# Performance work log

Measured on AMD Instinct MI355X. Metric: run time of the kernel, lower is better.

## Reference

```python
import jax, jax.numpy as jnp
import numpy as np

N_NODES = 100000


def gcn_conv(x, W, b, edge_index, n_nodes):
    # PyG GCNConv (default args): add self-loops, symmetric normalization,
    # linear transform first, then normalized scatter-add aggregation, then bias.
    h = x @ W  # [N, out]
    loop = jnp.arange(n_nodes, dtype=edge_index.dtype)
    row = jnp.concatenate([edge_index[0], loop])  # sources
    col = jnp.concatenate([edge_index[1], loop])  # targets
    deg = jax.ops.segment_sum(jnp.ones_like(col, dtype=h.dtype), col, num_segments=n_nodes)
    dinv = jnp.where(deg > 0, jax.lax.rsqrt(deg), 0.0)
    norm = dinv[row] * dinv[col]  # [E']
    msg = h[row] * norm[:, None]  # gather + scale
    out = jax.ops.segment_sum(msg, col, num_segments=n_nodes)  # scatter-add
    return out + b


def setup_inputs() -> dict:
    key = jax.random.key(0)
    k1, k2, k3, k4 = jax.random.split(key, 4)
    N, E, F, H, C = N_NODES, 3200000, 128, 16, 8
    x = jax.random.normal(k1, (N, F), dtype=jnp.float32)
    edge_index = jax.random.randint(k2, (2, E), 0, N, dtype=jnp.int64)
    W1 = jax.random.normal(k3, (F, H), dtype=jnp.float32) / np.sqrt(F)
    b1 = jnp.zeros((H,), dtype=jnp.float32)
    W2 = jax.random.normal(k4, (H, C), dtype=jnp.float32) / np.sqrt(H)
    b2 = jnp.zeros((C,), dtype=jnp.float32)
    return {"x": x, "edge_index": edge_index, "W1": W1, "b1": b1, "W2": W2, "b2": b2}


def reference(x, edge_index, W1, b1, W2, b2):
    n = x.shape[0]
    h = jax.nn.relu(gcn_conv(x, W1, b1, edge_index, n))
    # F.dropout(training=self.training) is identity in eval mode
    out = gcn_conv(h, W2, b2, edge_index, n)
    return jax.nn.log_softmax(out, axis=1)
```

## Files before the change

kernel.cpp:

```cpp
#include <hip/hip_runtime.h>
#include <hip/hip_fp16.h>

#define F_IN 128
#define H1   16
#define C2   8
#define BSHIFT 7
#define BNODES 128
#define MAXBUCK 1024
#define NBLK 256
#define CAP  6144
#define CHUNK_CAP 12800

__global__ __launch_bounds__(512) void binScatter2_kernel(
        const int* __restrict__ ei, int E, int chunk, int nbuck,
        int* __restrict__ bbcScan, int* __restrict__ stage) {
    __shared__ int h[MAXBUCK];
    __shared__ int sc[512];
    __shared__ unsigned short rnk[CHUNK_CAP];
    int t = threadIdx.x;
    int blk = blockIdx.x;
    int base = blk * chunk;
    int csize = max(0, min(chunk, E - base));
    int blkBase = base;

    for (int i = t; i < MAXBUCK; i += 512) h[i] = 0;
    __syncthreads();

    const int* colp = ei + E + base;
    const int* rowp = ei + base;
    bool al4 = ((E & 3) == 0) && ((base & 3) == 0) && ((csize & 3) == 0);
    bool fit = (csize <= CHUNK_CAP);

    if (al4) {
        const int4* cv = reinterpret_cast<const int4*>(colp);
        int nv = csize >> 2;
        if (fit) {
            for (int i = t; i < nv; i += 512) {
                int4 c4 = cv[i];
                rnk[4 * i + 0] = (unsigned short)atomicAdd(&h[c4.x >> BSHIFT], 1);
                rnk[4 * i + 1] = (unsigned short)atomicAdd(&h[c4.y >> BSHIFT], 1);
                rnk[4 * i + 2] = (unsigned short)atomicAdd(&h[c4.z >> BSHIFT], 1);
                rnk[4 * i + 3] = (unsigned short)atomicAdd(&h[c4.w >> BSHIFT], 1);
            }
        } else {
            for (int i = t; i < nv; i += 512) {
                int4 c4 = cv[i];
                atomicAdd(&h[c4.x >> BSHIFT], 1);
                atomicAdd(&h[c4.y >> BSHIFT], 1);
                atomicAdd(&h[c4.z >> BSHIFT], 1);
                atomicAdd(&h[c4.w >> BSHIFT], 1);
            }
        }
    } else {
        if (fit) {
            for (int i = t; i < csize; i += 512)
                rnk[i] = (unsigned short)atomicAdd(&h[colp[i] >> BSHIFT], 1);
        } else {
            for (int i = t; i < csize; i += 512) atomicAdd(&h[colp[i] >> BSHIFT], 1);
        }
    }
    __syncthreads();

    int e0 = h[2 * t], e1 = h[2 * t + 1];
    int psum = e0 + e1;
    sc[t] = psum;
    __syncthreads();
    for (int off = 1; off < 512; off <<= 1) {
        int tmp = (t >= off) ? sc[t - off] : 0;
        __syncthreads();
        sc[t] += tmp;
        __syncthreads();
    }
    int excl = sc[t] - psum;
    h[2 * t] = blkBase + excl;
    h[2 * t + 1] = blkBase + excl + e0;
    __syncthreads();

    for (int b = t; b < nbuck; b += 512)
        bbcScan[blk * nbuck + b] = h[b];
    __syncthreads();

    if (al4) {
        const int4* cv = reinterpret_cast<const int4*>(colp);
        const int4* rv = reinterpret_cast<const int4*>(rowp);
        int nv = csize >> 2;
        if (fit) {
            for (int i = t; i < nv; i += 512) {
                int4 c4 = cv[i];
                int4 r4 = rv[i];
                stage[h[c4.x >> BSHIFT] + (int)rnk[4 * i + 0]] = (r4.x << BSHIFT) | (c4.x & (BNODES - 1));
                stage[h[c4.y >> BSHIFT] + (int)rnk[4 * i + 1]] = (r4.y << BSHIFT) | (c4.y & (BNODES - 1));
                stage[h[c4.z >> BSHIFT] + (int)rnk[4 * i + 2]] = (r4.z << BSHIFT) | (c4.z & (BNODES - 1));
                stage[h[c4.w >> BSHIFT] + (int)rnk[4 * i + 3]] = (r4.w << BSHIFT) | (c4.w & (BNODES - 1));
            }
        } else {
            for (int i = t; i < nv; i += 512) {
                int4 c4 = cv[i];
                int4 r4 = rv[i];
                int p0 = atomicAdd(&h[c4.x >> BSHIFT], 1);
                stage[p0] = (r4.x << BSHIFT) | (c4.x & (BNODES - 1));
                int p1 = atomicAdd(&h[c4.y >> BSHIFT], 1);
                stage[p1] = (r4.y << BSHIFT) | (c4.y & (BNODES - 1));
                int p2 = atomicAdd(&h[c4.z >> BSHIFT], 1);
                stage[p2] = (r4.z << BSHIFT) | (c4.z & (BNODES - 1));
                int p3 = atomicAdd(&h[c4.w >> BSHIFT], 1);
                stage[p3] = (r4.w << BSHIFT) | (c4.w & (BNODES - 1));
            }
        }
    } else {
        if (fit) {
            for (int i = t; i < csize; i += 512) {
                int r = rowp[i];
                int c = colp[i];
                stage[h[c >> BSHIFT] + (int)rnk[i]] = (r << BSHIFT) | (c & (BNODES - 1));
            }
        } else {
            for (int i = t; i < csize; i += 512) {
                int r = rowp[i];
                int c = colp[i];
                int p = atomicAdd(&h[c >> BSHIFT], 1);
                stage[p] = (r << BSHIFT) | (c & (BNODES - 1));
            }
        }
    }
}

__global__ __launch_bounds__(NBLK) void sortCSR_kernel(
        const int* __restrict__ stage, const int* __restrict__ bbcScan,
        int E, int nbuck, int chunk, int* __restrict__ srt,
        int* __restrict__ nodePtr, float* __restrict__ dinv, int N) {
    __shared__ int ldsRec[CAP];
    __shared__ unsigned char ranks[CAP];
    __shared__ int pref[NBLK];
    __shared__ int cnt[BNODES];
    __shared__ int cur[BNODES];
    int b = blockIdx.x;
    int t = threadIdx.x;

    int winS = min(t * chunk, E);
    int runS = min(bbcScan[t * nbuck + b], E);
    int runE = (b + 1 < nbuck) ? bbcScan[t * nbuck + b + 1] : min((t + 1) * chunk, E);
    runE = min(runE, E);
    int sz = runE - runS;

    pref[t] = runS - winS;
    __syncthreads();
    for (int off = NBLK / 2; off > 0; off >>= 1) {
        if (t < off) pref[t] += pref[t + off];
        __syncthreads();
    }
    int bucketStart = pref[0];
    __syncthreads();

    pref[t] = sz;
    __syncthreads();
    for (int off = 1; off < NBLK; off <<= 1) {
        int tmp = (t >= off) ? pref[t - off] : 0;
        __syncthreads();
        pref[t] += tmp;
        __syncthreads();
    }
    int myOff = pref[t] - sz;
    int T = pref[NBLK - 1];

    if (t < BNODES) cnt[t] = 0;
    __syncthreads();

    bool fit = (T <= CAP);
    if (fit) {
        for (int i = 0; i < sz; ++i) {
            int rec = stage[runS + i];
            ldsRec[myOff + i] = rec;
            ranks[myOff + i] = (unsigned char)atomicAdd(&cnt[rec & (BNODES - 1)], 1);
        }
    } else {
        for (int i = runS; i < runE; ++i)
            atomicAdd(&cnt[stage[i] & (BNODES - 1)], 1);
    }
    __syncthreads();

    if (t < BNODES) cur[t] = cnt[t];
    __syncthreads();
    for (int off = 1; off < BNODES; off <<= 1) {
        int tmp = 0;
        if (t < BNODES && t >= off) tmp = cur[t - off];
        __syncthreads();
        if (t < BNODES) cur[t] += tmp;
        __syncthreads();
    }
    if (t < BNODES) {
        int excl = cur[t] - cnt[t];
        int v = b * BNODES + t;
        if (v < N) {
            nodePtr[v] = bucketStart + excl;
            dinv[v] = rsqrtf((float)cnt[t] + 1.0f);
        }
        cur[t] = bucketStart + excl;
    }
    if (b == nbuck - 1 && t == 0) nodePtr[N] = E;
    __syncthreads();

    if (fit) {
        for (int i = 0; i < sz; ++i) {
            int rec = ldsRec[myOff + i];
            srt[cur[rec & (BNODES - 1)] + (int)ranks[myOff + i]] = rec >> BSHIFT;
        }
    } else {
        for (int i = runS; i < runE; ++i) {
            int rec = stage[i];
            int p = atomicAdd(&cur[rec & (BNODES - 1)], 1);
            srt[p] = rec >> BSHIFT;
        }
    }
}

__global__ void gemm1_kernel(const float* __restrict__ x, const float* __restrict__ W1,
                             const float* __restrict__ dinv, __half* __restrict__ h1h, int N) {
    __shared__ float sW[F_IN * H1];
    for (int i = threadIdx.x; i < F_IN * H1; i += blockDim.x) sW[i] = W1[i];
    __syncthreads();
    int v = blockIdx.x * blockDim.x + threadIdx.x;
    if (v >= N) return;
    float acc[H1];
#pragma unroll
    for (int j = 0; j < H1; ++j) acc[j] = 0.0f;
    const float4* xr = reinterpret_cast<const float4*>(x + (size_t)v * F_IN);
#pragma unroll 8
    for (int k4 = 0; k4 < F_IN / 4; ++k4) {
        float4 xv = xr[k4];
        const float* w = &sW[k4 * 4 * H1];
#pragma unroll
        for (int j = 0; j < H1; ++j) acc[j] += xv.x * w[j];
#pragma unroll
        for (int j = 0; j < H1; ++j) acc[j] += xv.y * w[H1 + j];
#pragma unroll
        for (int j = 0; j < H1; ++j) acc[j] += xv.z * w[2 * H1 + j];
#pragma unroll
        for (int j = 0; j < H1; ++j) acc[j] += xv.w * w[3 * H1 + j];
    }
    float di = dinv[v];
    alignas(16) __half2 hp[8];
#pragma unroll
    for (int q = 0; q < 8; ++q)
        hp[q] = __floats2half2_rn(acc[2 * q] * di, acc[2 * q + 1] * di);
    float4* ho = reinterpret_cast<float4*>(h1h + (size_t)v * H1);
    ho[0] = *reinterpret_cast<float4*>(&hp[0]);
    ho[1] = *reinterpret_cast<float4*>(&hp[4]);
}

#define AGG1_TB 512
__global__ __launch_bounds__(AGG1_TB) void agg1_kernel(
        const int* __restrict__ srt, const int* __restrict__ nodePtr,
        const __half* __restrict__ h1h, const float* __restrict__ dinv,
        const float* __restrict__ b1, const float* __restrict__ W2,
        __half* __restrict__ h2h, int N) {
    __shared__ float hrelu[BNODES][H1 + 1];
    __shared__ float sW[H1 * C2];
    __shared__ float sb[H1];
    for (int i = threadIdx.x; i < H1 * C2; i += AGG1_TB) sW[i] = W2[i];
    for (int i = threadIdx.x; i < H1; i += AGG1_TB) sb[i] = b1[i];
    __syncthreads();

    int base = blockIdx.x * BNODES;
    int vi = threadIdx.x >> 2;
    int ep = (threadIdx.x >> 1) & 1;
    int q  = threadIdx.x & 1;
    int v  = base + vi;

    if (v < N) {
        int p  = nodePtr[v];
        int pe = nodePtr[v + 1];
        float a0[8], a1[8];
#pragma unroll
        for (int k = 0; k < 8; ++k) { a0[k] = 0.f; a1[k] = 0.f; }
        int e = p + ep;
        for (; e + 2 < pe; e += 4) {
            int r0 = srt[e];
            int r1 = srt[e + 2];
            float4 p0 = *reinterpret_cast<const float4*>(h1h + (size_t)r0 * H1 + q * 8);
            float4 p1 = *reinterpret_cast<const float4*>(h1h + (size_t)r1 * H1 + q * 8);
            const __half2* h0 = reinterpret_cast<const __half2*>(&p0);
            const __half2* h1_ = reinterpret_cast<const __half2*>(&p1);
#pragma unroll
            for (int k = 0; k < 4; ++k) {
                float2 f0 = __half22float2(h0[k]);
                float2 f1 = __half22float2(h1_[k]);
                a0[2 * k] += f0.x; a0[2 * k + 1] += f0.y;
                a1[2 * k] += f1.x; a1[2 * k + 1] += f1.y;
            }
        }
        for (; e < pe; e += 2) {
            int r0 = srt[e];
            float4 p0 = *reinterpret_cast<const float4*>(h1h + (size_t)r0 * H1 + q * 8);
            const __half2* h0 = reinterpret_cast<const __half2*>(&p0);
#pragma unroll
            for (int k = 0; k < 4; ++k) {
                float2 f0 = __half22float2(h0[k]);
                a0[2 * k] += f0.x; a0[2 * k + 1] += f0.y;
            }
        }
#pragma unroll
        for (int k = 0; k < 8; ++k) a0[k] += a1[k];
#pragma unroll
        for (int k = 0; k < 8; ++k) a0[k] += __shfl_xor(a0[k], 2);

        if (ep == 0) {
            float4 ps = *reinterpret_cast<const float4*>(h1h + (size_t)v * H1 + q * 8);
            const __half2* hs = reinterpret_cast<const __half2*>(&ps);
            float di = dinv[v];
#pragma unroll
            for (int k = 0; k < 4; ++k) {
                float2 fs = __half22float2(hs[k]);
                int j0 = q * 8 + 2 * k, j1 = j0 + 1;
                hrelu[vi][j0] = fmaxf(di * (a0[2 * k] + fs.x) + sb[j0], 0.0f);
                hrelu[vi][j1] = fmaxf(di * (a0[2 * k + 1] + fs.y) + sb[j1], 0.0f);
            }
        }
    }
    __syncthreads();

    int j = threadIdx.x & 7;
    for (int vi2 = threadIdx.x >> 3; vi2 < BNODES; vi2 += (AGG1_TB >> 3)) {
        int v2 = base + vi2;
        if (v2 < N) {
            float dot = 0.0f;
#pragma unroll
            for (int k = 0; k < H1; ++k) dot += hrelu[vi2][k] * sW[k * C2 + j];
            h2h[(size_t)v2 * C2 + j] = __float2half(dot * dinv[v2]);
        }
    }
}

#define AGG2_TB 256
__global__ __launch_bounds__(AGG2_TB) void agg2_kernel(
        const int* __restrict__ srt, const int* __restrict__ nodePtr,
        const __half* __restrict__ h2h, const float* __restrict__ dinv,
        const float* __restrict__ b2, float* __restrict__ out, int N) {
    int vi  = threadIdx.x >> 1;
    int par = threadIdx.x & 1;
    int v = blockIdx.x * (AGG2_TB / 2) + vi;
    if (v >= N) return;
    int p  = nodePtr[v];
    int pe = nodePtr[v + 1];
    float a0[8], a1[8];
#pragma unroll
    for (int k = 0; k < 8; ++k) { a0[k] = 0.f; a1[k] = 0.f; }
    int e = p + par;
    for (; e + 2 < pe; e += 4) {
        int r0 = srt[e];
        int r1 = srt[e + 2];
        float4 p0 = *reinterpret_cast<const float4*>(h2h + (size_t)r0 * C2);
        float4 p1 = *reinterpret_cast<const float4*>(h2h + (size_t)r1 * C2);
        const __half2* h0 = reinterpret_cast<const __half2*>(&p0);
        const __half2* h1_ = reinterpret_cast<const __half2*>(&p1);
#pragma unroll
        for (int k = 0; k < 4; ++k) {
            float2 f0 = __half22float2(h0[k]);
            float2 f1 = __half22float2(h1_[k]);
            a0[2 * k] += f0.x; a0[2 * k + 1] += f0.y;
            a1[2 * k] += f1.x; a1[2 * k + 1] += f1.y;
        }
    }
    for (; e < pe; e += 2) {
        int r0 = srt[e];
        float4 p0 = *reinterpret_cast<const float4*>(h2h + (size_t)r0 * C2);
        const __half2* h0 = reinterpret_cast<const __half2*>(&p0);
#pragma unroll
        for (int k = 0; k < 4; ++k) {
            float2 f0 = __half22float2(h0[k]);
            a0[2 * k] += f0.x; a0[2 * k + 1] += f0.y;
        }
    }
#pragma unroll
    for (int k = 0; k < 8; ++k) a0[k] += a1[k];
#pragma unroll
    for (int k = 0; k < 8; ++k) a0[k] += __shfl_xor(a0[k], 1);
    if (par) return;

    float4 ps = *reinterpret_cast<const float4*>(h2h + (size_t)v * C2);
    const __half2* hs = reinterpret_cast<const __half2*>(&ps);
    float di = dinv[v];
    float z[C2];
#pragma unroll
    for (int k = 0; k < 4; ++k) {
        float2 fs = __half22float2(hs[k]);
        z[2 * k]     = di * (a0[2 * k] + fs.x) + b2[2 * k];
        z[2 * k + 1] = di * (a0[2 * k + 1] + fs.y) + b2[2 * k + 1];
    }
    float m = z[0];
#pragma unroll
    for (int j = 1; j < C2; ++j) m = fmaxf(m, z[j]);
    float s = 0.0f;
#pragma unroll
    for (int j = 0; j < C2; ++j) s += __expf(z[j] - m);
    float lse = m + logf(s);
    float4* o = reinterpret_cast<float4*>(out + (size_t)v * C2);
    o[0] = make_float4(z[0] - lse, z[1] - lse, z[2] - lse, z[3] - lse);
    o[1] = make_float4(z[4] - lse, z[5] - lse, z[6] - lse, z[7] - lse);
}

extern "C" void kernel_launch(void* const* d_in, const int* in_sizes, int n_in,
                              void* d_out, int out_size, void* d_ws, size_t ws_size,
                              hipStream_t stream) {
    const float* x  = (const float*)d_in[0];
    const int*   ei = (const int*)d_in[1];
    const float* W1 = (const float*)d_in[2];
    const float* b1 = (const float*)d_in[3];
    const float* W2 = (const float*)d_in[4];
    const float* b2 = (const float*)d_in[5];
    float* out = (float*)d_out;

    const int N = in_sizes[0] / F_IN;
    const int E = in_sizes[1] / 2;
    const int nbuck = (N + BNODES - 1) >> BSHIFT;
    const int M = NBLK * nbuck;
    int chunk = (E + NBLK - 1) / NBLK;
    chunk = (chunk + 3) & ~3;

    int*    stage   = (int*)d_ws;
    int*    srt     = stage + E;
    int*    bbcScan = srt + E;
    int*    nodePtr = bbcScan + M;
    float*  dinv    = (float*)(nodePtr + N + 8);
    __half* h1h     = (__half*)(dinv + N);
    __half* h2h     = h1h + (size_t)16 * N;

    const int TB = 256;

    binScatter2_kernel<<<NBLK, 512, 0, stream>>>(ei, E, chunk, nbuck, bbcScan, stage);
    sortCSR_kernel<<<nbuck, NBLK, 0, stream>>>(stage, bbcScan, E, nbuck, chunk, srt, nodePtr, dinv, N);
    gemm1_kernel<<<(N + TB - 1) / TB, TB, 0, stream>>>(x, W1, dinv, h1h, N);
    agg1_kernel<<<nbuck, AGG1_TB, 0, stream>>>(srt, nodePtr, h1h, dinv, b1, W2, h2h, N);
    agg2_kernel<<<(N + (AGG2_TB / 2) - 1) / (AGG2_TB / 2), AGG2_TB, 0, stream>>>(srt, nodePtr, h2h, dinv, b2, out, N);
}
```

Before: 127.7 us.

## Fuse GEMM1 into edge binning kernel and apply source dinv during aggregation

The first-layer GEMM moves into extra blocks of the edge-binning kernel, so it no longer depends on dinv and can run alongside the scatter phase, which removes one kernel launch. The source-degree normalization moves out of the GEMM output and into agg1, which now loads dinv[r] per edge and does an extra multiply per element. This trades a serialized GEMM pass for more random gathers in the aggregation loop. The GEMM blocks reuse the rnk shared buffer for W1, and the kernel shares 512-thread launch bounds with the binning blocks.

```diff
diff --git a/kernel.cpp b/kernel.cpp
--- a/kernel.cpp
+++ b/kernel.cpp
@@ -11,13 +11,49 @@
 #define CAP  6144
 #define CHUNK_CAP 12800
 
-__global__ __launch_bounds__(512) void binScatter2_kernel(
+__global__ __launch_bounds__(512) void binGemm_kernel(
         const int* __restrict__ ei, int E, int chunk, int nbuck,
-        int* __restrict__ bbcScan, int* __restrict__ stage) {
+        int* __restrict__ bbcScan, int* __restrict__ stage,
+        const float* __restrict__ x, const float* __restrict__ W1,
+        __half* __restrict__ h1u, int N) {
     __shared__ int h[MAXBUCK];
     __shared__ int sc[512];
     __shared__ unsigned short rnk[CHUNK_CAP];
     int t = threadIdx.x;
+
+    if (blockIdx.x >= NBLK) {
+        float* sW = reinterpret_cast<float*>(rnk);
+        for (int i = t; i < F_IN * H1; i += 512) sW[i] = W1[i];
+        __syncthreads();
+        int v = (blockIdx.x - NBLK) * 512 + t;
+        if (v >= N) return;
+        float acc[H1];
+#pragma unroll
+        for (int j = 0; j < H1; ++j) acc[j] = 0.0f;
+        const float4* xr = reinterpret_cast<const float4*>(x + (size_t)v * F_IN);
+#pragma unroll 8
+        for (int k4 = 0; k4 < F_IN / 4; ++k4) {
+            float4 xv = xr[k4];
+            const float* w = &sW[k4 * 4 * H1];
+#pragma unroll
+            for (int j = 0; j < H1; ++j) acc[j] += xv.x * w[j];
+#pragma unroll
+            for (int j = 0; j < H1; ++j) acc[j] += xv.y * w[H1 + j];
+#pragma unroll
+            for (int j = 0; j < H1; ++j) acc[j] += xv.z * w[2 * H1 + j];
+#pragma unroll
+            for (int j = 0; j < H1; ++j) acc[j] += xv.w * w[3 * H1 + j];
+        }
+        alignas(16) __half2 hp[8];
+#pragma unroll
+        for (int q = 0; q < 8; ++q)
+            hp[q] = __floats2half2_rn(acc[2 * q], acc[2 * q + 1]);
+        float4* ho = reinterpret_cast<float4*>(h1u + (size_t)v * H1);
+        ho[0] = *reinterpret_cast<float4*>(&hp[0]);
+        ho[1] = *reinterpret_cast<float4*>(&hp[4]);
+        return;
+    }
+
     int blk = blockIdx.x;
     int base = blk * chunk;
     int csize = max(0, min(chunk, E - base));
@@ -214,44 +250,10 @@
     }
 }
 
-__global__ void gemm1_kernel(const float* __restrict__ x, const float* __restrict__ W1,
-                             const float* __restrict__ dinv, __half* __restrict__ h1h, int N) {
-    __shared__ float sW[F_IN * H1];
-    for (int i = threadIdx.x; i < F_IN * H1; i += blockDim.x) sW[i] = W1[i];
-    __syncthreads();
-    int v = blockIdx.x * blockDim.x + threadIdx.x;
-    if (v >= N) return;
-    float acc[H1];
-#pragma unroll
-    for (int j = 0; j < H1; ++j) acc[j] = 0.0f;
-    const float4* xr = reinterpret_cast<const float4*>(x + (size_t)v * F_IN);
-#pragma unroll 8
-    for (int k4 = 0; k4 < F_IN / 4; ++k4) {
-        float4 xv = xr[k4];
-        const float* w = &sW[k4 * 4 * H1];
-#pragma unroll
-        for (int j = 0; j < H1; ++j) acc[j] += xv.x * w[j];
-#pragma unroll
-        for (int j = 0; j < H1; ++j) acc[j] += xv.y * w[H1 + j];
-#pragma unroll
-        for (int j = 0; j < H1; ++j) acc[j] += xv.z * w[2 * H1 + j];
-#pragma unroll
-        for (int j = 0; j < H1; ++j) acc[j] += xv.w * w[3 * H1 + j];
-    }
-    float di = dinv[v];
-    alignas(16) __half2 hp[8];
-#pragma unroll
-    for (int q = 0; q < 8; ++q)
-        hp[q] = __floats2half2_rn(acc[2 * q] * di, acc[2 * q + 1] * di);
-    float4* ho = reinterpret_cast<float4*>(h1h + (size_t)v * H1);
-    ho[0] = *reinterpret_cast<float4*>(&hp[0]);
-    ho[1] = *reinterpret_cast<float4*>(&hp[4]);
-}
-
 #define AGG1_TB 512
 __global__ __launch_bounds__(AGG1_TB) void agg1_kernel(
         const int* __restrict__ srt, const int* __restrict__ nodePtr,
-        const __half* __restrict__ h1h, const float* __restrict__ dinv,
+        const __half* __restrict__ h1u, const float* __restrict__ dinv,
         const float* __restrict__ b1, const float* __restrict__ W2,
         __half* __restrict__ h2h, int N) {
     __shared__ float hrelu[BNODES][H1 + 1];
@@ -277,26 +279,29 @@
         for (; e + 2 < pe; e += 4) {
             int r0 = srt[e];
             int r1 = srt[e + 2];
-            float4 p0 = *reinterpret_cast<const float4*>(h1h + (size_t)r0 * H1 + q * 8);
-            float4 p1 = *reinterpret_cast<const float4*>(h1h + (size_t)r1 * H1 + q * 8);
+            float d0 = dinv[r0];
+            float d1 = dinv[r1];
+            float4 p0 = *reinterpret_cast<const float4*>(h1u + (size_t)r0 * H1 + q * 8);
+            float4 p1 = *reinterpret_cast<const float4*>(h1u + (size_t)r1 * H1 + q * 8);
             const __half2* h0 = reinterpret_cast<const __half2*>(&p0);
             const __half2* h1_ = reinterpret_cast<const __half2*>(&p1);
 #pragma unroll
             for (int k = 0; k < 4; ++k) {
                 float2 f0 = __half22float2(h0[k]);
                 float2 f1 = __half22float2(h1_[k]);
-                a0[2 * k] += f0.x; a0[2 * k + 1] += f0.y;
-                a1[2 * k] += f1.x; a1[2 * k + 1] += f1.y;
+                a0[2 * k] += d0 * f0.x; a0[2 * k + 1] += d0 * f0.y;
+                a1[2 * k] += d1 * f1.x; a1[2 * k + 1] += d1 * f1.y;
             }
         }
         for (; e < pe; e += 2) {
             int r0 = srt[e];
-            float4 p0 = *reinterpret_cast<const float4*>(h1h + (size_t)r0 * H1 + q * 8);
+            float d0 = dinv[r0];
+            float4 p0 = *reinterpret_cast<const float4*>(h1u + (size_t)r0 * H1 + q * 8);
             const __half2* h0 = reinterpret_cast<const __half2*>(&p0);
 #pragma unroll
             for (int k = 0; k < 4; ++k) {
                 float2 f0 = __half22float2(h0[k]);
-                a0[2 * k] += f0.x; a0[2 * k + 1] += f0.y;
+                a0[2 * k] += d0 * f0.x; a0[2 * k + 1] += d0 * f0.y;
             }
         }
 #pragma unroll
@@ -305,15 +310,15 @@
         for (int k = 0; k < 8; ++k) a0[k] += __shfl_xor(a0[k], 2);
 
         if (ep == 0) {
-            float4 ps = *reinterpret_cast<const float4*>(h1h + (size_t)v * H1 + q * 8);
+            float4 ps = *reinterpret_cast<const float4*>(h1u + (size_t)v * H1 + q * 8);
             const __half2* hs = reinterpret_cast<const __half2*>(&ps);
-            float di = dinv[v];
+            float dv = dinv[v];
 #pragma unroll
             for (int k = 0; k < 4; ++k) {
                 float2 fs = __half22float2(hs[k]);
                 int j0 = q * 8 + 2 * k, j1 = j0 + 1;
-                hrelu[vi][j0] = fmaxf(di * (a0[2 * k] + fs.x) + sb[j0], 0.0f);
-                hrelu[vi][j1] = fmaxf(di * (a0[2 * k + 1] + fs.y) + sb[j1], 0.0f);
+                hrelu[vi][j0] = fmaxf(dv * (a0[2 * k] + dv * fs.x) + sb[j0], 0.0f);
+                hrelu[vi][j1] = fmaxf(dv * (a0[2 * k + 1] + dv * fs.y) + sb[j1], 0.0f);
             }
         }
     }
@@ -422,14 +427,14 @@
     int*    bbcScan = srt + E;
     int*    nodePtr = bbcScan + M;
     float*  dinv    = (float*)(nodePtr + N + 8);
-    __half* h1h     = (__half*)(dinv + N);
-    __half* h2h     = h1h + (size_t)16 * N;
-
-    const int TB = 256;
-
-    binScatter2_kernel<<<NBLK, 512, 0, stream>>>(ei, E, chunk, nbuck, bbcScan, stage);
+    __half* h1u     = (__half*)(dinv + N);
+    __half* h2h     = h1u + (size_t)16 * N;
+
+    const int gemmBlocks = (N + 511) / 512;
+
+    binGemm_kernel<<<NBLK + gemmBlocks, 512, 0, stream>>>(ei, E, chunk, nbuck,
+                                                          bbcScan, stage, x, W1, h1u, N);
     sortCSR_kernel<<<nbuck, NBLK, 0, stream>>>(stage, bbcScan, E, nbuck, chunk, srt, nodePtr, dinv, N);
-    gemm1_kernel<<<(N + TB - 1) / TB, TB, 0, stream>>>(x, W1, dinv, h1h, N);
-    agg1_kernel<<<nbuck, AGG1_TB, 0, stream>>>(srt, nodePtr, h1h, dinv, b1, W2, h2h, N);
+    agg1_kernel<<<nbuck, AGG1_TB, 0, stream>>>(srt, nodePtr, h1u, dinv, b1, W2, h2h, N);
     agg2_kernel<<<(N + (AGG2_TB / 2) - 1) / (AGG2_TB / 2), AGG2_TB, 0, stream>>>(srt, nodePtr, h2h, dinv, b2, out, N);
 }
```

After: 137.2 us. 1.07x slower.
